# Optimization experiments

Measured on AMD Instinct MI355X. Metric: run time of the kernel, lower is better.

## Reference

```python
import jax, jax.numpy as jnp
import numpy as np

IMG_W, IMG_H = 416.0, 416.0
NUM_CLASSES = 80
NUM_ANCH = 3
LABEL_SMOOTH = 0.0
IGNORE_THR = 0.5
EPS = 1e-7


def _iou_cxcywh(b1, b2):
    # boxes (cx,cy,w,h); broadcasting IoU
    b1_min = b1[..., :2] - b1[..., 2:4] * 0.5
    b1_max = b1[..., :2] + b1[..., 2:4] * 0.5
    b2_min = b2[..., :2] - b2[..., 2:4] * 0.5
    b2_max = b2[..., :2] + b2[..., 2:4] * 0.5
    inter_wh = jnp.clip(jnp.minimum(b1_max, b2_max) - jnp.maximum(b1_min, b2_min), 0.0)
    inter = inter_wh[..., 0] * inter_wh[..., 1]
    a1 = b1[..., 2] * b1[..., 3]
    a2 = b2[..., 2] * b2[..., 3]
    return inter / jnp.maximum(a1 + a2 - inter, EPS)


def _ciou(b1, b2):
    iou = _iou_cxcywh(b1, b2)
    center_d = jnp.sum((b1[..., :2] - b2[..., :2]) ** 2, -1)
    enc_min = jnp.minimum(b1[..., :2] - b1[..., 2:4] * 0.5, b2[..., :2] - b2[..., 2:4] * 0.5)
    enc_max = jnp.maximum(b1[..., :2] + b1[..., 2:4] * 0.5, b2[..., :2] + b2[..., 2:4] * 0.5)
    diag = jnp.sum((enc_max - enc_min) ** 2, -1)
    ciou = iou - center_d / jnp.maximum(diag, EPS)
    v = (4.0 / (np.pi ** 2)) * (jnp.arctan(b1[..., 2] / jnp.maximum(b1[..., 3], EPS))
                                - jnp.arctan(b2[..., 2] / jnp.maximum(b2[..., 3], EPS))) ** 2
    alpha = v / jnp.maximum(1.0 - iou + v, EPS)
    return ciou - alpha * v


def _decode_level(feat, anch_wh):
    # head_process for one level: sigmoid xy + grid, exp wh * anchor, sigmoid conf
    bs, ch, H, W = feat.shape
    A = anch_wh.shape[0]
    f = feat.reshape(bs, A, ch // A, H, W).transpose(0, 3, 4, 1, 2)  # [bs,H,W,A,5+C]
    sx, sy = IMG_W / W, IMG_H / H
    gx = jnp.arange(W, dtype=feat.dtype)[None, :, None]
    gy = jnp.arange(H, dtype=feat.dtype)[:, None, None]
    px = (jax.nn.sigmoid(f[..., 0]) + gx) * sx
    py = (jax.nn.sigmoid(f[..., 1]) + gy) * sy
    pw = jnp.exp(f[..., 2]) * anch_wh[:, 0]
    ph = jnp.exp(f[..., 3]) * anch_wh[:, 1]
    box = jnp.stack([px, py, pw, ph], -1).reshape(bs, H * W * A, 4)
    conf = jax.nn.sigmoid(f[..., 4]).reshape(bs, H * W * A)
    cls = f[..., 5:].reshape(bs, H * W * A, NUM_CLASSES)
    # anchor prior boxes at every cell, same (y,x,a) flatten order
    acx = jnp.broadcast_to((gx + 0.5) * sx, (H, W, A))
    acy = jnp.broadcast_to((gy + 0.5) * sy, (H, W, A))
    aw = jnp.broadcast_to(anch_wh[:, 0], (H, W, A))
    ah = jnp.broadcast_to(anch_wh[:, 1], (H, W, A))
    priors = jnp.stack([acx, acy, aw, ah], -1).reshape(H * W * A, 4)
    return box, conf, cls, priors


def _forward(feats0, feats1, feats2, targets, anchors_shape):
    feats = [feats0, feats1, feats2]
    bs, n_t = targets.shape[0], targets.shape[1]
    boxes, confs, clss, priors, sizes, offs = [], [], [], [], [], []
    off = 0
    for i, f in enumerate(feats):
        aw = anchors_shape[i * NUM_ANCH:(i + 1) * NUM_ANCH]
        b, c, cl, pr = _decode_level(f, aw)
        boxes.append(b); confs.append(c); clss.append(cl); priors.append(pr)
        H, W = f.shape[2], f.shape[3]
        sizes.append((W, H)); offs.append(off); off += H * W * NUM_ANCH
    pred_box = jnp.concatenate(boxes, 1)      # [bs, total, 4]
    conf = jnp.concatenate(confs, 1)          # [bs, total]
    pred_cls = jnp.concatenate(clss, 1)       # [bs, total, C]
    anchors_all = jnp.concatenate(priors, 0)  # [total, 4]
    total = pred_box.shape[1]

    # ---- match_obj: best anchor shape per target via wh-only IoU ----
    tw, th = targets[..., 2], targets[..., 3]
    aw_, ah_ = anchors_shape[:, 0], anchors_shape[:, 1]
    inter = jnp.minimum(tw[..., None], aw_) * jnp.minimum(th[..., None], ah_)
    shape_iou = inter / jnp.maximum(tw[..., None] * th[..., None] + aw_ * ah_ - inter, EPS)
    best = jnp.argmax(shape_iou, -1)          # [bs, n_t]
    level = best // NUM_ANCH
    a = (best % NUM_ANCH).astype(jnp.int32)
    fs = jnp.array(sizes, dtype=jnp.int32)    # [3, (W,H)]
    offs_arr = jnp.array(offs, dtype=jnp.int32)
    Wl = fs[level, 0].astype(targets.dtype)
    Hl = fs[level, 1].astype(targets.dtype)
    X = jnp.clip(jnp.floor(targets[..., 0] / IMG_W * Wl), 0, Wl - 1).astype(jnp.int32)
    Y = jnp.clip(jnp.floor(targets[..., 1] / IMG_H * Hl), 0, Hl - 1).astype(jnp.int32)
    flat = offs_arr[level] + (Y * fs[level, 0] + X) * NUM_ANCH + a
    bidx = jnp.broadcast_to(jnp.arange(bs)[:, None], (bs, n_t))
    tidx = jnp.arange(bs * n_t, dtype=jnp.int32).reshape(bs, n_t)
    obj_mask = jnp.full((bs, total), -1, jnp.int32).at[bidx, flat].set(tidx)
    noobj_mask = jnp.ones((bs, total), jnp.int32).at[bidx, flat].set(0)

    # ---- match_noobj: ignore priors overlapping any GT above threshold ----
    iou_tn = _iou_cxcywh(targets[:, :, None, :4], anchors_all[None, None, :, :])  # [bs,n_t,total]
    max_iou = jnp.max(iou_tn, 1)
    noobj_mask = jnp.where(max_iou > IGNORE_THR, 0, noobj_mask)

    # ---- confidence BCE ----
    obj_labels = (obj_mask >= 0).astype(conf.dtype)
    p = jnp.clip(conf, EPS, 1.0 - EPS)
    bce = -(obj_labels * jnp.log(p) + (1.0 - obj_labels) * jnp.log(1.0 - p))
    loss_conf = jnp.sum(bce * obj_labels) + jnp.sum(bce * noobj_mask.astype(conf.dtype))

    # ---- localization (CIoU) + classification (smoothed log-softmax) on positives ----
    pos = obj_labels
    tsel = targets.reshape(bs * n_t, 5)[jnp.clip(obj_mask, 0)]  # [bs,total,5]
    tb = tsel[..., :4]
    scale = 2.0 - tb[..., 2] / IMG_W * tb[..., 3] / IMG_H
    loss_loc = jnp.sum((1.0 - _ciou(pred_box, tb)) * scale * pos)
    logsm = jax.nn.log_softmax(pred_cls, -1)
    labels = tsel[..., 4].astype(jnp.int32)
    picked = jnp.take_along_axis(logsm, labels[..., None], -1)[..., 0]
    s = LABEL_SMOOTH
    cls_nll = -((1.0 - s) * picked + (s / NUM_CLASSES) * jnp.sum(logsm, -1))
    loss_cls = jnp.sum(cls_nll * pos)

    return (loss_conf + loss_cls + loss_loc) / bs


def setup_inputs():
    key = jax.random.key(0)
    ks = jax.random.split(key, 6)
    bs, n_t = 32, 20
    ch = NUM_ANCH * (5 + NUM_CLASSES)  # 255
    feats0 = jax.random.normal(ks[0], (bs, ch, 13, 13), jnp.float32) * 0.1
    feats1 = jax.random.normal(ks[1], (bs, ch, 26, 26), jnp.float32) * 0.1
    feats2 = jax.random.normal(ks[2], (bs, ch, 52, 52), jnp.float32) * 0.1
    cxy = jax.random.uniform(ks[3], (bs, n_t, 2), jnp.float32, 8.0, 408.0)
    wh = jax.random.uniform(ks[4], (bs, n_t, 2), jnp.float32, 8.0, 120.0)
    cls = jax.random.randint(ks[5], (bs, n_t, 1), 0, NUM_CLASSES).astype(jnp.float32)
    targets = jnp.concatenate([cxy, wh, cls], -1)  # (cx,cy,w,h,class) in pixels
    anchors_shape = jnp.array([[116, 90], [156, 198], [373, 326],
                               [30, 61], [62, 45], [59, 119],
                               [10, 13], [16, 30], [33, 23]], jnp.float32)
    return {"feats0": feats0, "feats1": feats1, "feats2": feats2,
            "targets": targets, "anchors_shape": anchors_shape}


def reference(feats0, feats1, feats2, targets, anchors_shape):
    return _forward(feats0, feats1, feats2, targets, anchors_shape)
```

## Files before the change

### kernel.cpp

```cpp
#include <hip/hip_runtime.h>
#include <math.h>

#define NUM_CLASSES 80
#define EPSF 1e-7f

constexpr int BS = 32;
constexpr int NT = 20;
constexpr int TOTAL_CELLS = 169 + 676 + 2704;
constexpr int TOTAL_POS   = TOTAL_CELLS * 3;
constexpr int THREADS     = 512;
constexpr int CONF_BLKS_PER_B = (TOTAL_POS + THREADS - 1) / THREADS;
constexpr int CONF_BLKS = CONF_BLKS_PER_B * BS;
constexpr int POS_BLKS  = (BS * NT) / 8;
constexpr int NBLK = CONF_BLKS + POS_BLKS;

__device__ __forceinline__ float sigmoidf_(float x) {
    return 1.0f / (1.0f + expf(-x));
}

__device__ __forceinline__ int target_flat(float tx, float ty, float tw, float th,
                                           const float* anch) {
    int best = 0; float bestv = -1.0f;
    #pragma unroll
    for (int k = 0; k < 9; ++k) {
        float aw = anch[2 * k], ah = anch[2 * k + 1];
        float inter = fminf(tw, aw) * fminf(th, ah);
        float v = inter / fmaxf(tw * th + aw * ah - inter, EPSF);
        if (v > bestv) { bestv = v; best = k; }
    }
    int lvl = best / 3, a = best - lvl * 3;
    int Wl  = (lvl == 0) ? 13 : ((lvl == 1) ? 26 : 52);
    int off = (lvl == 0) ? 0  : ((lvl == 1) ? 507 : 2535);
    float Wf = (float)Wl;
    int X = (int)floorf(tx / 416.0f * Wf);
    int Y = (int)floorf(ty / 416.0f * Wf);
    X = min(max(X, 0), Wl - 1);
    Y = min(max(Y, 0), Wl - 1);
    return off + (Y * Wl + X) * 3 + a;
}

__global__ __launch_bounds__(THREADS) void yolo_fused(
    const float* __restrict__ f0, const float* __restrict__ f1,
    const float* __restrict__ f2, const float* __restrict__ tgt,
    const float* __restrict__ anch, double* __restrict__ part)
{
    __shared__ double s_w[8];
    const int bi  = blockIdx.x;
    const int tid = threadIdx.x;
    double lsum = 0.0;

    if (bi < CONF_BLKS) {
        __shared__ float s_t[NT][5];
        __shared__ float s_anch[18];
        __shared__ int   s_flat[NT];
        const int b   = bi / CONF_BLKS_PER_B;
        const int sub = bi - b * CONF_BLKS_PER_B;

        if (tid < NT * 5) ((float*)s_t)[tid] = tgt[b * NT * 5 + tid];
        if (tid >= 128 && tid < 128 + 18) s_anch[tid - 128] = anch[tid - 128];
        __syncthreads();
        if (tid < NT)
            s_flat[tid] = target_flat(s_t[tid][0], s_t[tid][1], s_t[tid][2], s_t[tid][3], s_anch);
        __syncthreads();

        const int idx = sub * THREADS + tid;
        if (idx < TOTAL_POS) {
            const int a    = idx / TOTAL_CELLS;
            const int cell = idx - a * TOTAL_CELLS;
            int lvl, W, cell0, posoff;
            const float* __restrict__ fb;
            if (cell < 169)      { lvl = 0; W = 13; cell0 = 0;   posoff = 0;    fb = f0; }
            else if (cell < 845) { lvl = 1; W = 26; cell0 = 169; posoff = 507;  fb = f1; }
            else                 { lvl = 2; W = 52; cell0 = 845; posoff = 2535; fb = f2; }
            const int HW  = W * W;
            const int rel = cell - cell0;
            const int y   = rel / W;
            const int x   = rel - y * W;
            const int pos = posoff + rel * 3 + a;

            const float cl = fb[((size_t)b * 255 + a * 85 + 4) * HW + rel];
            float p = sigmoidf_(cl);
            p = fminf(fmaxf(p, EPSF), 1.0f - EPSF);

            bool assigned = false;
            #pragma unroll
            for (int n = 0; n < NT; ++n) assigned |= (s_flat[n] == pos);

            if (assigned) {
                lsum = -(double)logf(p);
            } else {
                const float sxy = 416.0f / (float)W;
                const float acx = ((float)x + 0.5f) * sxy;
                const float acy = ((float)y + 0.5f) * sxy;
                const float aw  = s_anch[(lvl * 3 + a) * 2];
                const float ah  = s_anch[(lvl * 3 + a) * 2 + 1];
                const float anx = acx - aw * 0.5f, axx = acx + aw * 0.5f;
                const float any_ = acy - ah * 0.5f, axy = acy + ah * 0.5f;
                const float aarea = aw * ah;
                float mx = 0.0f;
                #pragma unroll 4
                for (int n = 0; n < NT; ++n) {
                    float tbx = s_t[n][0], tby = s_t[n][1];
                    float tbw = s_t[n][2], tbh = s_t[n][3];
                    float iw = fmaxf(fminf(axx, tbx + tbw * 0.5f) - fmaxf(anx, tbx - tbw * 0.5f), 0.0f);
                    float ih = fmaxf(fminf(axy, tby + tbh * 0.5f) - fmaxf(any_, tby - tbh * 0.5f), 0.0f);
                    float inter = iw * ih;
                    mx = fmaxf(mx, inter / fmaxf(aarea + tbw * tbh - inter, EPSF));
                }
                if (!(mx > 0.5f)) lsum = -(double)logf(1.0f - p);
            }
        }
    } else {
        const int wv   = (bi - CONF_BLKS) * 8 + (tid >> 6);
        const int lane = tid & 63;
        const int b = wv / NT;
        const int t = wv - b * NT;

        float an[18];
        #pragma unroll
        for (int k = 0; k < 18; ++k) an[k] = anch[k];

        int my_flat = 0x7fffffff;
        if (lane < NT) {
            const float* tp = tgt + ((size_t)b * NT + lane) * 5;
            my_flat = target_flat(tp[0], tp[1], tp[2], tp[3], an);
        }
        const int flat_t = __shfl(my_flat, t);
        bool winner = true;
        for (int n = t + 1; n < NT; ++n)
            if (__shfl(my_flat, n) == flat_t) winner = false;

        if (winner) {
            int lvl, W, off;
            const float* __restrict__ fb;
            if (flat_t < 507)       { lvl = 0; W = 13; off = 0;    fb = f0; }
            else if (flat_t < 2535) { lvl = 1; W = 26; off = 507;  fb = f1; }
            else                    { lvl = 2; W = 52; off = 2535; fb = f2; }
            const int HW  = W * W;
            const int rel = (flat_t - off) / 3;
            const int a   = flat_t - off - rel * 3;
            const int y   = rel / W;
            const int x   = rel - y * W;
            const float* f = fb + ((size_t)b * 255 + a * 85) * HW + rel;

            const float* tp = tgt + ((size_t)b * NT + t) * 5;
            const float tbx = tp[0], tby = tp[1], tbw = tp[2], tbh = tp[3];
            const int  label = (int)tp[4];

            const int c1 = lane;
            const int c2 = 64 + lane;
            const float lg1 = f[(size_t)(5 + c1) * HW];
            const float lg2 = (c2 < NUM_CLASSES) ? f[(size_t)(5 + c2) * HW] : -1e30f;
            float m = fmaxf(lg1, lg2);
            #pragma unroll
            for (int s = 32; s > 0; s >>= 1) m = fmaxf(m, __shfl_xor(m, s));
            float ssum = expf(lg1 - m) + ((c2 < NUM_CLASSES) ? expf(lg2 - m) : 0.0f);
            float pick = (c1 == label ? lg1 : 0.0f) + (c2 == label ? lg2 : 0.0f);
            #pragma unroll
            for (int s = 32; s > 0; s >>= 1) {
                ssum += __shfl_xor(ssum, s);
                pick += __shfl_xor(pick, s);
            }
            if (lane == 0) {
                lsum = -(double)(pick - m - logf(ssum));

                const float sxy = 416.0f / (float)W;
                const float aw = an[(lvl * 3 + a) * 2], ah = an[(lvl * 3 + a) * 2 + 1];
                float px = (sigmoidf_(f[0])              + (float)x) * sxy;
                float py = (sigmoidf_(f[(size_t)HW])     + (float)y) * sxy;
                float pw = expf(f[(size_t)2 * HW]) * aw;
                float ph = expf(f[(size_t)3 * HW]) * ah;

                float b1nx = px - pw * 0.5f, b1xx = px + pw * 0.5f;
                float b1ny = py - ph * 0.5f, b1xy = py + ph * 0.5f;
                float b2nx = tbx - tbw * 0.5f, b2xx = tbx + tbw * 0.5f;
                float b2ny = tby - tbh * 0.5f, b2xy = tby + tbh * 0.5f;
                float iw = fmaxf(fminf(b1xx, b2xx) - fmaxf(b1nx, b2nx), 0.0f);
                float ih = fmaxf(fminf(b1xy, b2xy) - fmaxf(b1ny, b2ny), 0.0f);
                float inter = iw * ih;
                float iou = inter / fmaxf(pw * ph + tbw * tbh - inter, EPSF);
                float cd = (px - tbx) * (px - tbx) + (py - tby) * (py - tby);
                float enx = fminf(b1nx, b2nx), exx = fmaxf(b1xx, b2xx);
                float eny = fminf(b1ny, b2ny), exy = fmaxf(b1xy, b2xy);
                float diag = (exx - enx) * (exx - enx) + (exy - eny) * (exy - eny);
                float ciou = iou - cd / fmaxf(diag, EPSF);
                float dA = atanf(pw / fmaxf(ph, EPSF)) - atanf(tbw / fmaxf(tbh, EPSF));
                float v = (4.0f / (float)(M_PI * M_PI)) * dA * dA;
                float alpha = v / fmaxf(1.0f - iou + v, EPSF);
                float scale = 2.0f - tbw / 416.0f * tbh / 416.0f;
                lsum += (double)((1.0f - (ciou - alpha * v)) * scale);
            }
        }
    }

    #pragma unroll
    for (int s = 32; s > 0; s >>= 1) lsum += __shfl_xor(lsum, s);
    if ((tid & 63) == 0) s_w[tid >> 6] = lsum;
    __syncthreads();
    if (tid == 0) {
        double v = 0.0;
        #pragma unroll
        for (int w = 0; w < 8; ++w) v += s_w[w];
        part[bi] = v;
    }
}

__global__ __launch_bounds__(256) void yolo_finish(const double* __restrict__ part,
                                                   float* __restrict__ out)
{
    __shared__ double s_w[4];
    const int tid = threadIdx.x;
    double v = 0.0;
    for (int i = tid; i < NBLK; i += 256) v += part[i];
    #pragma unroll
    for (int s = 32; s > 0; s >>= 1) v += __shfl_xor(v, s);
    if ((tid & 63) == 0) s_w[tid >> 6] = v;
    __syncthreads();
    if (tid == 0) out[0] = (float)((s_w[0] + s_w[1] + s_w[2] + s_w[3]) / (double)BS);
}

extern "C" void kernel_launch(void* const* d_in, const int* in_sizes, int n_in,
                              void* d_out, int out_size, void* d_ws, size_t ws_size,
                              hipStream_t stream) {
    const float* f0   = (const float*)d_in[0];
    const float* f1   = (const float*)d_in[1];
    const float* f2   = (const float*)d_in[2];
    const float* tgt  = (const float*)d_in[3];
    const float* anch = (const float*)d_in[4];
    double* part = (double*)d_ws;

    yolo_fused<<<NBLK, THREADS, 0, stream>>>(f0, f1, f2, tgt, anch, part);
    yolo_finish<<<1, 256, 0, stream>>>(part, (float*)d_out);
}
```

Before: 18.91 us.

## Replace finish kernel with atomic accumulation and prefetch conf logit before syncs

Removes the second reduction kernel: each block now atomically adds its scaled partial sum directly into the zeroed output, which is cleared with a memset. It also issues the per-thread confidence-logit global load before the shared-memory setup and barriers so the load latency overlaps the target assignment work. The trade is a memset node plus float atomics whose ordering is nondeterministic, giving slightly different rounding than the double-precision two-stage reduction.

```diff
diff --git a/kernel.cpp b/kernel.cpp
--- a/kernel.cpp
+++ b/kernel.cpp
@@ -42,7 +42,7 @@
 __global__ __launch_bounds__(THREADS) void yolo_fused(
     const float* __restrict__ f0, const float* __restrict__ f1,
     const float* __restrict__ f2, const float* __restrict__ tgt,
-    const float* __restrict__ anch, double* __restrict__ part)
+    const float* __restrict__ anch, float* __restrict__ out)
 {
     __shared__ double s_w[8];
     const int bi  = blockIdx.x;
@@ -56,6 +56,20 @@
         const int b   = bi / CONF_BLKS_PER_B;
         const int sub = bi - b * CONF_BLKS_PER_B;
 
+        const int idx = sub * THREADS + tid;
+        const bool valid = idx < TOTAL_POS;
+        int a = 0, cell = 0, lvl = 0, W = 13, cell0 = 0, posoff = 0;
+        const float* __restrict__ fb = f0;
+        float cl = 0.0f;
+        if (valid) {
+            a    = idx / TOTAL_CELLS;
+            cell = idx - a * TOTAL_CELLS;
+            if (cell < 169)      { lvl = 0; W = 13; cell0 = 0;   posoff = 0;    fb = f0; }
+            else if (cell < 845) { lvl = 1; W = 26; cell0 = 169; posoff = 507;  fb = f1; }
+            else                 { lvl = 2; W = 52; cell0 = 845; posoff = 2535; fb = f2; }
+            cl = fb[((size_t)b * 255 + a * 85 + 4) * (W * W) + (cell - cell0)];
+        }
+
         if (tid < NT * 5) ((float*)s_t)[tid] = tgt[b * NT * 5 + tid];
         if (tid >= 128 && tid < 128 + 18) s_anch[tid - 128] = anch[tid - 128];
         __syncthreads();
@@ -63,22 +77,13 @@
             s_flat[tid] = target_flat(s_t[tid][0], s_t[tid][1], s_t[tid][2], s_t[tid][3], s_anch);
         __syncthreads();
 
-        const int idx = sub * THREADS + tid;
-        if (idx < TOTAL_POS) {
-            const int a    = idx / TOTAL_CELLS;
-            const int cell = idx - a * TOTAL_CELLS;
-            int lvl, W, cell0, posoff;
-            const float* __restrict__ fb;
-            if (cell < 169)      { lvl = 0; W = 13; cell0 = 0;   posoff = 0;    fb = f0; }
-            else if (cell < 845) { lvl = 1; W = 26; cell0 = 169; posoff = 507;  fb = f1; }
-            else                 { lvl = 2; W = 52; cell0 = 845; posoff = 2535; fb = f2; }
+        if (valid) {
             const int HW  = W * W;
             const int rel = cell - cell0;
             const int y   = rel / W;
             const int x   = rel - y * W;
             const int pos = posoff + rel * 3 + a;
 
-            const float cl = fb[((size_t)b * 255 + a * 85 + 4) * HW + rel];
             float p = sigmoidf_(cl);
             p = fminf(fmaxf(p, EPSF), 1.0f - EPSF);
 
@@ -201,22 +206,8 @@
         double v = 0.0;
         #pragma unroll
         for (int w = 0; w < 8; ++w) v += s_w[w];
-        part[bi] = v;
+        atomicAdd(out, (float)(v / (double)BS));
     }
-}
-
-__global__ __launch_bounds__(256) void yolo_finish(const double* __restrict__ part,
-                                                   float* __restrict__ out)
-{
-    __shared__ double s_w[4];
-    const int tid = threadIdx.x;
-    double v = 0.0;
-    for (int i = tid; i < NBLK; i += 256) v += part[i];
-    #pragma unroll
-    for (int s = 32; s > 0; s >>= 1) v += __shfl_xor(v, s);
-    if ((tid & 63) == 0) s_w[tid >> 6] = v;
-    __syncthreads();
-    if (tid == 0) out[0] = (float)((s_w[0] + s_w[1] + s_w[2] + s_w[3]) / (double)BS);
 }
 
 extern "C" void kernel_launch(void* const* d_in, const int* in_sizes, int n_in,
@@ -227,8 +218,7 @@
     const float* f2   = (const float*)d_in[2];
     const float* tgt  = (const float*)d_in[3];
     const float* anch = (const float*)d_in[4];
-    double* part = (double*)d_ws;
-
-    yolo_fused<<<NBLK, THREADS, 0, stream>>>(f0, f1, f2, tgt, anch, part);
-    yolo_finish<<<1, 256, 0, stream>>>(part, (float*)d_out);
-}
+
+    hipMemsetAsync(d_out, 0, sizeof(float), stream);
+    yolo_fused<<<NBLK, THREADS, 0, stream>>>(f0, f1, f2, tgt, anch, (float*)d_out);
+}
```

Result: slower. 24.89 us (+31.6%).
